# Performance work log

Measured on AMD Instinct MI355X. Metric: run time of the kernel, lower is better.

Reference implementation:

```python
import jax, jax.numpy as jnp
import numpy as np

N = 100000      # nodes
E = 600000      # directed edges (reciprocal pairs)
D_NODE = 128    # node feature dim (== hidden, required by torch.where broadcast)
D_BOND = 16     # bond feature dim
HID = 128       # hidden size
DEPTH = 3       # message passing depth


def setup_inputs() -> dict:
    key = jax.random.key(0)
    ks = jax.random.split(key, 8)
    x = jax.random.normal(ks[0], (N, D_NODE), jnp.float32)
    # build edges as reciprocal pairs: edge 2i = (u,v), edge 2i+1 = (v,u)
    half = E // 2
    u = jax.random.randint(ks[1], (half,), 0, N)
    v = jax.random.randint(ks[2], (half,), 0, N)
    src = jnp.stack([u, v], axis=1).reshape(-1)
    dst = jnp.stack([v, u], axis=1).reshape(-1)
    edge_index = jnp.stack([src, dst])          # [2, E]
    rev_edge_index = jnp.arange(E) ^ 1           # reverse edge of 2i is 2i+1
    edge_attr = jax.random.normal(ks[3], (E, D_BOND), jnp.float32)
    # learned params (Linear: y = x @ W + b)
    s_i = 1.0 / np.sqrt(D_NODE + D_BOND)
    s_h = 1.0 / np.sqrt(HID)
    s_o = 1.0 / np.sqrt(D_NODE + HID)
    W_i = jax.random.normal(ks[4], (D_NODE + D_BOND, HID), jnp.float32) * s_i
    b_i = jnp.zeros((HID,), jnp.float32)
    W_h = jax.random.normal(ks[5], (HID, HID), jnp.float32) * s_h
    b_h = jnp.zeros((HID,), jnp.float32)
    W_o = jax.random.normal(ks[6], (D_NODE + HID, HID), jnp.float32) * s_o
    b_o = jnp.zeros((HID,), jnp.float32)
    return dict(x=x, edge_attr=edge_attr, W_i=W_i, b_i=b_i, W_h=W_h, b_h=b_h,
                W_o=W_o, b_o=b_o, edge_index=edge_index,
                rev_edge_index=rev_edge_index)


def reference(x, edge_attr, W_i, b_i, W_h, b_h, W_o, b_o,
              edge_index, rev_edge_index):
    src, dst = edge_index[0], edge_index[1]
    # H_0 = relu(W_i([x[src]; edge_attr]))
    H0 = jax.nn.relu(jnp.concatenate([x[src], edge_attr], axis=1) @ W_i + b_i)
    H = H0
    for _ in range(DEPTH - 1):
        # message: scatter-sum over dst, gather by src, subtract reverse edge
        agg = jax.ops.segment_sum(H, dst, num_segments=N)   # [N, HID]
        M = agg[src] - H[rev_edge_index]                    # [E, HID]
        # update: relu(H0 + W_h(M))   (dropout is identity in eval)
        H = jax.nn.relu(H0 + M @ W_h + b_h)
    # final node aggregation
    Mn = jax.ops.segment_sum(H, dst, num_segments=N)        # [N, HID]
    Mn = jnp.where(jnp.sum(Mn, axis=1, keepdims=True) == 0, x, Mn)
    out = jax.nn.relu(jnp.concatenate([x, Mn], axis=1) @ W_o + b_o)  # [N, HID]
    return out
```

## Files before the change

kernel.cpp:

```cpp
#include <hip/hip_runtime.h>
#include <hip/hip_bf16.h>

#define N_NODES 100000
#define N_EDGES 600000
#define HID 128
#define D_BOND 16
#define NB_CHUNKS 98

typedef __attribute__((ext_vector_type(8))) short bf16x8;
typedef __attribute__((ext_vector_type(4))) float f32x4;

__device__ __forceinline__ float bf2f(unsigned int u) {
    return __uint_as_float((u & 0xffffu) << 16);
}
__device__ __forceinline__ unsigned short f2bf(float f) {
    unsigned int x = __float_as_uint(f);
    x += 0x7fffu + ((x >> 16) & 1u);
    return (unsigned short)(x >> 16);
}
__device__ __forceinline__ unsigned int pk2(float a, float b) {
    return (unsigned int)f2bf(a) | ((unsigned int)f2bf(b) << 16);
}

template<int STRIDE, int XM>
__device__ __forceinline__ void stw(unsigned char* tile, int row, int byte, uint4 v) {
    *reinterpret_cast<uint4*>(tile + ((row * STRIDE + byte) ^ ((row & XM) << 4))) = v;
}
template<int STRIDE, int XM>
__device__ __forceinline__ uint4 ldw(const unsigned char* tile, int row, int byte) {
    return *reinterpret_cast<const uint4*>(tile + ((row * STRIDE + byte) ^ ((row & XM) << 4)));
}
template<int STRIDE, int XM>
__device__ __forceinline__ bf16x8 lda(const unsigned char* tile, int row, int byte) {
    return *reinterpret_cast<const bf16x8*>(tile + ((row * STRIDE + byte) ^ ((row & XM) << 4)));
}
template<int STRIDE, int XM>
__device__ __forceinline__ void st2w(unsigned char* tile, int row, int col, unsigned short v) {
    *reinterpret_cast<unsigned short*>(tile + ((row * STRIDE + col * 2) ^ ((row & XM) << 4))) = v;
}

__device__ __forceinline__ bf16x8 ifrag(int l, int shift) {
    bf16x8 b;
    const int target = (l & 15) + shift;
#pragma unroll
    for (int j = 0; j < 8; ++j)
        b[j] = (short)((((l >> 4) * 8 + j) == target) ? 0x3F80 : 0);
    return b;
}

__global__ __launch_bounds__(256) void k_hist(const int* __restrict__ dst,
                                              int* __restrict__ cnt) {
    int e = blockIdx.x * 256 + threadIdx.x;
    if (e < N_EDGES) atomicAdd(&cnt[dst[e]], 1);
}

__global__ __launch_bounds__(256) void k_blocksum(const int* __restrict__ cnt,
                                                  int* __restrict__ bsum) {
    __shared__ int red[256];
    const int b = blockIdx.x, t = threadIdx.x;
    const int base = b * 1024 + t * 4;
    int s = 0;
#pragma unroll
    for (int i = 0; i < 4; ++i) { int n = base + i; if (n < N_NODES) s += cnt[n]; }
    red[t] = s; __syncthreads();
    for (int o = 128; o > 0; o >>= 1) { if (t < o) red[t] += red[t + o]; __syncthreads(); }
    if (t == 0) bsum[b] = red[0];
}

__global__ __launch_bounds__(128) void k_scan_bsum(const int* __restrict__ bsum,
                                                   int* __restrict__ boff,
                                                   int* __restrict__ rowptr) {
    __shared__ int s[128];
    const int t = threadIdx.x;
    const int v = (t < NB_CHUNKS) ? bsum[t] : 0;
    s[t] = v; __syncthreads();
    for (int o = 1; o < 128; o <<= 1) {
        int add = 0; if (t >= o) add = s[t - o];
        __syncthreads();
        s[t] += add; __syncthreads();
    }
    if (t < NB_CHUNKS) boff[t] = s[t] - v;
    if (t == 0) rowptr[N_NODES] = N_EDGES;
}

__global__ __launch_bounds__(256) void k_scan_chunk(const int* __restrict__ cnt,
                                                    const int* __restrict__ boff,
                                                    int* __restrict__ rowptr,
                                                    int* __restrict__ wpos) {
    __shared__ int s[256];
    const int b = blockIdx.x, t = threadIdx.x;
    const int base = b * 1024 + t * 4;
    int v[4]; int ts = 0;
#pragma unroll
    for (int i = 0; i < 4; ++i) { int n = base + i; v[i] = (n < N_NODES) ? cnt[n] : 0; ts += v[i]; }
    s[t] = ts; __syncthreads();
    for (int o = 1; o < 256; o <<= 1) {
        int add = 0; if (t >= o) add = s[t - o];
        __syncthreads();
        s[t] += add; __syncthreads();
    }
    int run = s[t] - ts + boff[b];
#pragma unroll
    for (int i = 0; i < 4; ++i) {
        int n = base + i;
        if (n < N_NODES) { rowptr[n] = run; wpos[n] = run; }
        run += v[i];
    }
}

__global__ __launch_bounds__(256) void k_fill(const int* __restrict__ dst,
                                              int* __restrict__ wpos,
                                              int* __restrict__ eidx) {
    int e = blockIdx.x * 256 + threadIdx.x;
    if (e < N_EDGES) { int p = atomicAdd(&wpos[dst[e]], 1); eidx[p] = e; }
}

__global__ __launch_bounds__(256) void k_eacvt(const float* __restrict__ ea,
                                               unsigned short* __restrict__ eabf) {
    const size_t i = (size_t)(blockIdx.x * 256 + threadIdx.x) * 8;
    if (i >= (size_t)N_EDGES * D_BOND) return;
    const float4 v0 = *reinterpret_cast<const float4*>(&ea[i]);
    const float4 v1 = *reinterpret_cast<const float4*>(&ea[i + 4]);
    uint4 o;
    o.x = pk2(v0.x, v0.y); o.y = pk2(v0.z, v0.w);
    o.z = pk2(v1.x, v1.y); o.w = pk2(v1.z, v1.w);
    *reinterpret_cast<uint4*>(&eabf[i]) = o;
}

__global__ __launch_bounds__(256) void k_pack(const float* __restrict__ Wi,
                                              const float* __restrict__ Wh,
                                              const float* __restrict__ Wo,
                                              unsigned short* __restrict__ Pie,
                                              unsigned short* __restrict__ Pix,
                                              unsigned short* __restrict__ Ph,
                                              unsigned short* __restrict__ PhN,
                                              unsigned short* __restrict__ Po) {
    const int tid = blockIdx.x * 256 + threadIdx.x;
    const float* W; unsigned short* P; int Krows, base; float sgn = 1.f;
    if (tid < 512)        { W = Wi + 128 * HID; P = Pie; Krows = 16;  base = tid; }
    else if (tid < 2560)  { W = Wi; P = Pix; Krows = 128; base = tid - 512; }
    else if (tid < 4608)  { W = Wh; P = Ph;  Krows = 128; base = tid - 2560; }
    else if (tid < 6656)  { W = Wh; P = PhN; Krows = 128; base = tid - 4608; sgn = -1.f; }
    else                  { W = Wo; P = Po;  Krows = 256; base = tid - 6656; }
    const int l = base & 63, fc = base >> 6;
    const int c = fc & 7, kk = fc >> 3;
    const int col = c * 16 + (l & 15);
    const int k0 = kk * 32 + (l >> 4) * 8;
    float v[8];
#pragma unroll
    for (int j = 0; j < 8; ++j) {
        const int k = k0 + j;
        v[j] = (k < Krows) ? sgn * W[(size_t)k * HID + col] : 0.f;
    }
    uint4 o;
    o.x = pk2(v[0], v[1]); o.y = pk2(v[2], v[3]);
    o.z = pk2(v[4], v[5]); o.w = pk2(v[6], v[7]);
    *reinterpret_cast<uint4*>(&P[(size_t)base * 8]) = o;
}

__global__ __launch_bounds__(256) void k_xw(const float* __restrict__ x,
                                            const unsigned short* __restrict__ Pix,
                                            void* __restrict__ xa) {
    __shared__ __align__(16) unsigned char tX[32 * 256];
    const int n0 = blockIdx.x * 32;
    const int t = threadIdx.x;
#pragma unroll
    for (int i = 0; i < 2; ++i) {
        const int f = t + 256 * i, row = f >> 4, u = f & 15;
        const float* xp = &x[(size_t)(n0 + row) * HID + u * 8];
        const float4 v0 = *reinterpret_cast<const float4*>(xp);
        const float4 v1 = *reinterpret_cast<const float4*>(xp + 4);
        uint4 o;
        o.x = pk2(v0.x, v0.y); o.y = pk2(v0.z, v0.w);
        o.z = pk2(v1.x, v1.y); o.w = pk2(v1.z, v1.w);
        stw<256, 7>(tX, row, u * 16, o);
    }
    __syncthreads();
    const int w = t >> 6, l = t & 63;
    const int wr = w & 1, cb = (w >> 1) * 4;
    const int arow = 16 * wr + (l & 15);
    const int ko = (l >> 4) * 16;
    f32x4 acc[4] = {};
#pragma unroll
    for (int kk = 0; kk < 4; ++kk) {
        const bf16x8 a = lda<256, 7>(tX, arow, kk * 64 + ko);
#pragma unroll
        for (int c = 0; c < 4; ++c) {
            const bf16x8 b = *reinterpret_cast<const bf16x8*>(&Pix[(((kk * 8) + cb + c) * 64 + l) * 8]);
            acc[c] = __builtin_amdgcn_mfma_f32_16x16x32_bf16(a, b, acc[c], 0, 0, 0);
        }
    }
    __syncthreads();
    const int rbase = 16 * wr + 4 * (l >> 4);
#pragma unroll
    for (int c = 0; c < 4; ++c) {
        const int col = ((cb + c) << 4) | (l & 15);
#pragma unroll
        for (int rr = 0; rr < 4; ++rr)
            st2w<256, 7>(tX, rbase + rr, col, f2bf(acc[c][rr]));
    }
    __syncthreads();
#pragma unroll
    for (int i = 0; i < 2; ++i) {
        const int f = t + 256 * i, row = f >> 4, u = f & 15;
        *reinterpret_cast<uint4*>((char*)xa + (size_t)(n0 + row) * 512 + u * 16) =
            ldw<256, 7>(tX, row, u * 16);
    }
}

template<int STRIDE>
__device__ __forceinline__ void xw_init(const unsigned char* tX, int ar0, int ko,
                                        int cb, int l, f32x4 (&acc)[2][4]) {
    const bf16x8 bI0 = ifrag(l, 0), bI1 = ifrag(l, 16);
    const f32x4 z = {0.f, 0.f, 0.f, 0.f};
#pragma unroll
    for (int c = 0; c < 4; ++c) {
        const int fc = cb + c;
        const int wb = (fc == 7) ? 192 : 32 * fc;
        const bf16x8 bI = (fc == 7) ? bI1 : bI0;
        acc[0][c] = __builtin_amdgcn_mfma_f32_16x16x32_bf16(lda<STRIDE, 7>(tX, ar0, wb + ko), bI, z, 0, 0, 0);
        acc[1][c] = __builtin_amdgcn_mfma_f32_16x16x32_bf16(lda<STRIDE, 7>(tX, ar0 + 16, wb + ko), bI, z, 0, 0, 0);
    }
}

__global__ __launch_bounds__(256) void k_h0(const void* __restrict__ xa,
                                            const unsigned short* __restrict__ eabf,
                                            const unsigned short* __restrict__ Pie,
                                            const float* __restrict__ bi,
                                            const int* __restrict__ src,
                                            unsigned short* __restrict__ H) {
    __shared__ __align__(16) unsigned char tX[64 * 256];
    __shared__ __align__(16) unsigned char tE[64 * 64];
    __shared__ int s_src[64];
    const int e0 = blockIdx.x * 64;
    const int t = threadIdx.x;
    if (t < 64) s_src[t] = src[e0 + t];
    __syncthreads();
#pragma unroll
    for (int i = 0; i < 4; ++i) {
        const int f = t + 256 * i, e = f >> 4, u = f & 15;
        stw<256, 7>(tX, e, u * 16,
            *reinterpret_cast<const uint4*>((const char*)xa + (size_t)s_src[e] * 512 + u * 16));
    }
    {
        const int e = t >> 2, u = t & 3;
        uint4 v = make_uint4(0, 0, 0, 0);
        if (u < 2) v = *reinterpret_cast<const uint4*>(&eabf[(size_t)(e0 + e) * D_BOND + u * 8]);
        stw<64, 3>(tE, e, u * 16, v);
    }
    __syncthreads();
    const int w = t >> 6, l = t & 63;
    const int cb = (w & 1) * 4, wr0 = (w >> 1) * 2;
    const int ar0 = 16 * wr0 + (l & 15);
    const int ko = (l >> 4) * 16;
    f32x4 acc[2][4];
    xw_init<256>(tX, ar0, ko, cb, l, acc);
    {
        const bf16x8 a0 = lda<64, 3>(tE, ar0, ko);
        const bf16x8 a1 = lda<64, 3>(tE, ar0 + 16, ko);
#pragma unroll
        for (int c = 0; c < 4; ++c) {
            const bf16x8 b = *reinterpret_cast<const bf16x8*>(&Pie[((cb + c) * 64 + l) * 8]);
            acc[0][c] = __builtin_amdgcn_mfma_f32_16x16x32_bf16(a0, b, acc[0][c], 0, 0, 0);
            acc[1][c] = __builtin_amdgcn_mfma_f32_16x16x32_bf16(a1, b, acc[1][c], 0, 0, 0);
        }
    }
    __syncthreads();
#pragma unroll
    for (int r = 0; r < 2; ++r) {
        const int rbase = 16 * (wr0 + r) + 4 * (l >> 4);
#pragma unroll
        for (int c = 0; c < 4; ++c) {
            const int col = ((cb + c) << 4) | (l & 15);
            const float bv = bi[col];
#pragma unroll
            for (int rr = 0; rr < 4; ++rr)
                st2w<256, 7>(tX, rbase + rr, col, f2bf(fmaxf(acc[r][c][rr] + bv, 0.f)));
        }
    }
    __syncthreads();
#pragma unroll
    for (int i = 0; i < 4; ++i) {
        const int f = t + 256 * i, row = f >> 4, u = f & 15;
        *reinterpret_cast<uint4*>(&H[(size_t)(e0 + row) * HID + u * 8]) = ldw<256, 7>(tX, row, u * 16);
    }
}

__global__ __launch_bounds__(256) void k_agg(const unsigned short* __restrict__ H,
                                             const int* __restrict__ rowptr,
                                             const int* __restrict__ eidx,
                                             void* __restrict__ xa) {
    const int wid = (blockIdx.x * 256 + threadIdx.x) >> 6;
    const int lane = threadIdx.x & 63;
    if (wid >= N_NODES) return;
    const int beg = rowptr[wid], end = rowptr[wid + 1];
    float a0 = 0.f, a1 = 0.f;
    int j = beg;
    for (; j + 4 <= end; j += 4) {
        const int ei0 = eidx[j], ei1 = eidx[j + 1], ei2 = eidx[j + 2], ei3 = eidx[j + 3];
        const unsigned int p0 = *reinterpret_cast<const unsigned int*>(&H[(size_t)ei0 * HID + lane * 2]);
        const unsigned int p1 = *reinterpret_cast<const unsigned int*>(&H[(size_t)ei1 * HID + lane * 2]);
        const unsigned int p2 = *reinterpret_cast<const unsigned int*>(&H[(size_t)ei2 * HID + lane * 2]);
        const unsigned int p3 = *reinterpret_cast<const unsigned int*>(&H[(size_t)ei3 * HID + lane * 2]);
        a0 += bf2f(p0) + bf2f(p1) + bf2f(p2) + bf2f(p3);
        a1 += bf2f(p0 >> 16) + bf2f(p1 >> 16) + bf2f(p2 >> 16) + bf2f(p3 >> 16);
    }
    for (; j < end; ++j) {
        const int e = eidx[j];
        const unsigned int p = *reinterpret_cast<const unsigned int*>(&H[(size_t)e * HID + lane * 2]);
        a0 += bf2f(p);
        a1 += bf2f(p >> 16);
    }
    *reinterpret_cast<unsigned int*>((char*)xa + (size_t)wid * 512 + 256 + lane * 4) = pk2(a0, a1);
}

__global__ __launch_bounds__(256) void k_msg(const void* __restrict__ xa,
                                             const unsigned short* __restrict__ eabf,
                                             const unsigned short* __restrict__ Pie,
                                             const float* __restrict__ bi,
                                             const unsigned short* __restrict__ Ph,
                                             const unsigned short* __restrict__ PhN,
                                             const float* __restrict__ bh,
                                             const int* __restrict__ src,
                                             unsigned short* H) {
    __shared__ __align__(16) unsigned char tA[64 * 512];
    __shared__ __align__(16) unsigned char tH[64 * 256];
    __shared__ __align__(16) unsigned char tE[64 * 64];
    __shared__ int s_src[64];
    const int e0 = blockIdx.x * 64;
    const int t = threadIdx.x;
    if (t < 64) s_src[t] = src[e0 + t];
    __syncthreads();

#pragma unroll
    for (int i = 0; i < 8; ++i) {
        const int f = t + 256 * i, e = f >> 5, u = f & 31;
        stw<512, 7>(tA, e, u * 16,
            *reinterpret_cast<const uint4*>((const char*)xa + (size_t)s_src[e] * 512 + u * 16));
    }
#pragma unroll
    for (int i = 0; i < 4; ++i) {
        const int f = t + 256 * i, e = f >> 4, u = f & 15;
        stw<256, 7>(tH, e, u * 16,
            *reinterpret_cast<const uint4*>(&H[(size_t)((e0 + e) ^ 1) * HID + u * 8]));
    }
    {
        const int e = t >> 2, u = t & 3;
        uint4 v = make_uint4(0, 0, 0, 0);
        if (u < 2) v = *reinterpret_cast<const uint4*>(&eabf[(size_t)(e0 + e) * D_BOND + u * 8]);
        stw<64, 3>(tE, e, u * 16, v);
    }
    __syncthreads();

    const int w = t >> 6, l = t & 63;
    const int cb = (w & 1) * 4, wr0 = (w >> 1) * 2;
    const int ar0 = 16 * wr0 + (l & 15);
    const int ko = (l >> 4) * 16;

    f32x4 acc[2][4];
    xw_init<512>(tA, ar0, ko, cb, l, acc);
    {
        const bf16x8 a0 = lda<64, 3>(tE, ar0, ko);
        const bf16x8 a1 = lda<64, 3>(tE, ar0 + 16, ko);
#pragma unroll
        for (int c = 0; c < 4; ++c) {
            const bf16x8 b = *reinterpret_cast<const bf16x8*>(&Pie[((cb + c) * 64 + l) * 8]);
            acc[0][c] = __builtin_amdgcn_mfma_f32_16x16x32_bf16(a0, b, acc[0][c], 0, 0, 0);
            acc[1][c] = __builtin_amdgcn_mfma_f32_16x16x32_bf16(a1, b, acc[1][c], 0, 0, 0);
        }
    }
#pragma unroll
    for (int r = 0; r < 2; ++r)
#pragma unroll
        for (int c = 0; c < 4; ++c) {
            const float bv = bi[((cb + c) << 4) | (l & 15)];
#pragma unroll
            for (int rr = 0; rr < 4; ++rr) acc[r][c][rr] = fmaxf(acc[r][c][rr] + bv, 0.f);
        }
#pragma unroll
    for (int kk = 0; kk < 4; ++kk) {
        const bf16x8 a0 = lda<512, 7>(tA, ar0, 256 + kk * 64 + ko);
        const bf16x8 a1 = lda<512, 7>(tA, ar0 + 16, 256 + kk * 64 + ko);
#pragma unroll
        for (int c = 0; c < 4; ++c) {
            const bf16x8 b = *reinterpret_cast<const bf16x8*>(&Ph[(((kk * 8) + cb + c) * 64 + l) * 8]);
            acc[0][c] = __builtin_amdgcn_mfma_f32_16x16x32_bf16(a0, b, acc[0][c], 0, 0, 0);
            acc[1][c] = __builtin_amdgcn_mfma_f32_16x16x32_bf16(a1, b, acc[1][c], 0, 0, 0);
        }
    }
#pragma unroll
    for (int kk = 0; kk < 4; ++kk) {
        const bf16x8 a0 = lda<256, 7>(tH, ar0, kk * 64 + ko);
        const bf16x8 a1 = lda<256, 7>(tH, ar0 + 16, kk * 64 + ko);
#pragma unroll
        for (int c = 0; c < 4; ++c) {
            const bf16x8 b = *reinterpret_cast<const bf16x8*>(&PhN[(((kk * 8) + cb + c) * 64 + l) * 8]);
            acc[0][c] = __builtin_amdgcn_mfma_f32_16x16x32_bf16(a0, b, acc[0][c], 0, 0, 0);
            acc[1][c] = __builtin_amdgcn_mfma_f32_16x16x32_bf16(a1, b, acc[1][c], 0, 0, 0);
        }
    }
    __syncthreads();

#pragma unroll
    for (int r = 0; r < 2; ++r) {
        const int rbase = 16 * (wr0 + r) + 4 * (l >> 4);
#pragma unroll
        for (int c = 0; c < 4; ++c) {
            const int col = ((cb + c) << 4) | (l & 15);
            const float bv = bh[col];
#pragma unroll
            for (int rr = 0; rr < 4; ++rr)
                st2w<256, 7>(tH, rbase + rr, col, f2bf(fmaxf(acc[r][c][rr] + bv, 0.f)));
        }
    }
    __syncthreads();
#pragma unroll
    for (int i = 0; i < 4; ++i) {
        const int f = t + 256 * i, row = f >> 4, u = f & 15;
        *reinterpret_cast<uint4*>(&H[(size_t)(e0 + row) * HID + u * 8]) = ldw<256, 7>(tH, row, u * 16);
    }
}

__global__ __launch_bounds__(256) void k_out(const float* __restrict__ x,
                                             const void* xa,
                                             const int* __restrict__ cnt,
                                             const unsigned short* __restrict__ Po,
                                             const float* __restrict__ bo,
                                             float* out) {
    __shared__ __align__(16) unsigned char tile[32 * 512];
    __shared__ int s_cnt[32];
    const int n0 = blockIdx.x * 32;
    const int t = threadIdx.x;
    if (t < 32) s_cnt[t] = cnt[n0 + t];
    __syncthreads();
    for (int f = t; f < 1024; f += 256) {
        const int e = f >> 5, u = f & 31;
        uint4 o;
        if (u >= 16 && s_cnt[e] > 0) {
            o = *reinterpret_cast<const uint4*>((const char*)xa + (size_t)(n0 + e) * 512 + 256 + (u - 16) * 16);
        } else {
            const int k8 = (u & 15) * 8;
            const float* xp = &x[(size_t)(n0 + e) * HID + k8];
            const float4 v0 = *reinterpret_cast<const float4*>(xp);
            const float4 v1 = *reinterpret_cast<const float4*>(xp + 4);
            o.x = pk2(v0.x, v0.y); o.y = pk2(v0.z, v0.w);
            o.z = pk2(v1.x, v1.y); o.w = pk2(v1.z, v1.w);
        }
        stw<512, 7>(tile, e, u * 16, o);
    }
    __syncthreads();
    const int w = t >> 6, l = t & 63;
    const int wr = w & 1, cb = (w >> 1) * 4;
    const int arow = 16 * wr + (l & 15);
    const int ko = (l >> 4) * 16;
    f32x4 acc[4] = {};
#pragma unroll
    for (int kk = 0; kk < 8; ++kk) {
        const bf16x8 a = lda<512, 7>(tile, arow, kk * 64 + ko);
#pragma unroll
        for (int c = 0; c < 4; ++c) {
            const bf16x8 b = *reinterpret_cast<const bf16x8*>(&Po[(((kk * 8) + cb + c) * 64 + l) * 8]);
            acc[c] = __builtin_amdgcn_mfma_f32_16x16x32_bf16(a, b, acc[c], 0, 0, 0);
        }
    }
    const int frow = 16 * wr + 4 * (l >> 4);
#pragma unroll
    for (int c = 0; c < 4; ++c) {
        const int col = ((cb + c) << 4) | (l & 15);
        const float bias = bo[col];
#pragma unroll
        for (int r = 0; r < 4; ++r) {
            out[(size_t)(n0 + frow + r) * HID + col] = fmaxf(acc[c][r] + bias, 0.f);
        }
    }
}

extern "C" void kernel_launch(void* const* d_in, const int* in_sizes, int n_in,
                              void* d_out, int out_size, void* d_ws, size_t ws_size,
                              hipStream_t stream) {
    const float* x  = (const float*)d_in[0];
    const float* ea = (const float*)d_in[1];
    const float* Wi = (const float*)d_in[2];
    const float* bi = (const float*)d_in[3];
    const float* Wh = (const float*)d_in[4];
    const float* bh = (const float*)d_in[5];
    const float* Wo = (const float*)d_in[6];
    const float* bo = (const float*)d_in[7];
    const int* ei   = (const int*)d_in[8];
    const int* src  = ei;
    const int* dst  = ei + N_EDGES;

    char* ws = (char*)d_ws;
    size_t off = 0;
    auto alloc = [&](size_t bytes) -> void* {
        void* p = ws + off;
        off += (bytes + 255) & ~(size_t)255;
        return p;
    };
    unsigned short* H    = (unsigned short*)alloc((size_t)N_EDGES * HID * 2);
    unsigned short* eabf = (unsigned short*)alloc((size_t)N_EDGES * D_BOND * 2);
    int* cnt     = (int*)alloc((size_t)N_NODES * 4);
    int* rowptr  = (int*)alloc((size_t)(N_NODES + 1) * 4);
    int* wpos    = (int*)alloc((size_t)N_NODES * 4);
    int* bsum    = (int*)alloc(512);
    int* boff    = (int*)alloc(512);
    int* eidx    = (int*)alloc((size_t)N_EDGES * 4);
    unsigned short* Pie = (unsigned short*)alloc(512 * 8 * 2);
    unsigned short* Pix = (unsigned short*)alloc(2048 * 8 * 2);
    unsigned short* Ph  = (unsigned short*)alloc(2048 * 8 * 2);
    unsigned short* PhN = (unsigned short*)alloc(2048 * 8 * 2);
    unsigned short* Po  = (unsigned short*)alloc(4096 * 8 * 2);
    void* xa = d_out;

    const int EB = (N_EDGES + 255) / 256;

    hipMemsetAsync(cnt, 0, (size_t)N_NODES * 4, stream);
    k_hist<<<EB, 256, 0, stream>>>(dst, cnt);
    k_blocksum<<<NB_CHUNKS, 256, 0, stream>>>(cnt, bsum);
    k_scan_bsum<<<1, 128, 0, stream>>>(bsum, boff, rowptr);
    k_scan_chunk<<<NB_CHUNKS, 256, 0, stream>>>(cnt, boff, rowptr, wpos);
    k_fill<<<EB, 256, 0, stream>>>(dst, wpos, eidx);

    k_eacvt<<<(N_EDGES * D_BOND / 8 + 255) / 256, 256, 0, stream>>>(ea, eabf);
    k_pack<<<42, 256, 0, stream>>>(Wi, Wh, Wo, Pie, Pix, Ph, PhN, Po);
    k_xw<<<N_NODES / 32, 256, 0, stream>>>(x, Pix, xa);

    k_h0<<<N_EDGES / 64, 256, 0, stream>>>(xa, eabf, Pie, bi, src, H);

    k_agg<<<N_NODES / 4, 256, 0, stream>>>(H, rowptr, eidx, xa);
    k_msg<<<N_EDGES / 64, 256, 0, stream>>>(xa, eabf, Pie, bi, Ph, PhN, bh, src, H);

    k_agg<<<N_NODES / 4, 256, 0, stream>>>(H, rowptr, eidx, xa);
    k_msg<<<N_EDGES / 64, 256, 0, stream>>>(xa, eabf, Pie, bi, Ph, PhN, bh, src, H);

    k_agg<<<N_NODES / 4, 256, 0, stream>>>(H, rowptr, eidx, xa);
    k_out<<<N_NODES / 32, 256, 0, stream>>>(x, xa, cnt, Po, bo, (float*)d_out);
}
```

Before: 625.8 us.

## Recompute H0 on the fly and drop the separate H0 materialization kernel

Removes the k_h0 kernel that wrote the full edge-level H0 tensor. A new k_agg0 rebuilds H0 per incoming edge from the precomputed x·W_i rows plus the bond features, and sums it straight into the node aggregate. The first k_msg variant recomputes H0 in shared memory and reads each edge's reverse by XOR-ing the row inside the 64-edge tile, since reciprocal edges are adjacent. The later variant loads H rows contiguously and does the same XOR in LDS instead of gathering globally. This saves a full edge-tensor write and read, at the cost of redundant scalar FMA work and uncoalesced fp32 edge_attr reads in k_agg0.

```diff
diff --git a/kernel.cpp b/kernel.cpp
--- a/kernel.cpp
+++ b/kernel.cpp
@@ -223,67 +223,43 @@
     }
 }
 
-__global__ __launch_bounds__(256) void k_h0(const void* __restrict__ xa,
-                                            const unsigned short* __restrict__ eabf,
-                                            const unsigned short* __restrict__ Pie,
-                                            const float* __restrict__ bi,
-                                            const int* __restrict__ src,
-                                            unsigned short* __restrict__ H) {
-    __shared__ __align__(16) unsigned char tX[64 * 256];
-    __shared__ __align__(16) unsigned char tE[64 * 64];
-    __shared__ int s_src[64];
-    const int e0 = blockIdx.x * 64;
-    const int t = threadIdx.x;
-    if (t < 64) s_src[t] = src[e0 + t];
-    __syncthreads();
-#pragma unroll
-    for (int i = 0; i < 4; ++i) {
-        const int f = t + 256 * i, e = f >> 4, u = f & 15;
-        stw<256, 7>(tX, e, u * 16,
-            *reinterpret_cast<const uint4*>((const char*)xa + (size_t)s_src[e] * 512 + u * 16));
-    }
-    {
-        const int e = t >> 2, u = t & 3;
-        uint4 v = make_uint4(0, 0, 0, 0);
-        if (u < 2) v = *reinterpret_cast<const uint4*>(&eabf[(size_t)(e0 + e) * D_BOND + u * 8]);
-        stw<64, 3>(tE, e, u * 16, v);
-    }
-    __syncthreads();
-    const int w = t >> 6, l = t & 63;
-    const int cb = (w & 1) * 4, wr0 = (w >> 1) * 2;
-    const int ar0 = 16 * wr0 + (l & 15);
-    const int ko = (l >> 4) * 16;
-    f32x4 acc[2][4];
-    xw_init<256>(tX, ar0, ko, cb, l, acc);
-    {
-        const bf16x8 a0 = lda<64, 3>(tE, ar0, ko);
-        const bf16x8 a1 = lda<64, 3>(tE, ar0 + 16, ko);
-#pragma unroll
-        for (int c = 0; c < 4; ++c) {
-            const bf16x8 b = *reinterpret_cast<const bf16x8*>(&Pie[((cb + c) * 64 + l) * 8]);
-            acc[0][c] = __builtin_amdgcn_mfma_f32_16x16x32_bf16(a0, b, acc[0][c], 0, 0, 0);
-            acc[1][c] = __builtin_amdgcn_mfma_f32_16x16x32_bf16(a1, b, acc[1][c], 0, 0, 0);
-        }
-    }
-    __syncthreads();
-#pragma unroll
-    for (int r = 0; r < 2; ++r) {
-        const int rbase = 16 * (wr0 + r) + 4 * (l >> 4);
-#pragma unroll
-        for (int c = 0; c < 4; ++c) {
-            const int col = ((cb + c) << 4) | (l & 15);
-            const float bv = bi[col];
-#pragma unroll
-            for (int rr = 0; rr < 4; ++rr)
-                st2w<256, 7>(tX, rbase + rr, col, f2bf(fmaxf(acc[r][c][rr] + bv, 0.f)));
-        }
-    }
-    __syncthreads();
-#pragma unroll
-    for (int i = 0; i < 4; ++i) {
-        const int f = t + 256 * i, row = f >> 4, u = f & 15;
-        *reinterpret_cast<uint4*>(&H[(size_t)(e0 + row) * HID + u * 8]) = ldw<256, 7>(tX, row, u * 16);
-    }
+__global__ __launch_bounds__(256) void k_agg0(const int* __restrict__ rowptr,
+                                              const int* __restrict__ eidx,
+                                              const int* __restrict__ src,
+                                              const float* __restrict__ ea,
+                                              const float* __restrict__ Wi,
+                                              const float* __restrict__ bi,
+                                              void* __restrict__ xa) {
+    const int wid = (blockIdx.x * 256 + threadIdx.x) >> 6;
+    const int lane = threadIdx.x & 63;
+    if (wid >= N_NODES) return;
+    const int c0 = lane * 2;
+    float w2x[16], w2y[16];
+#pragma unroll
+    for (int k = 0; k < 16; ++k) {
+        const float2 v = *reinterpret_cast<const float2*>(&Wi[(size_t)(128 + k) * HID + c0]);
+        w2x[k] = v.x; w2y[k] = v.y;
+    }
+    const float2 bv = *reinterpret_cast<const float2*>(&bi[c0]);
+    float a0 = 0.f, a1 = 0.f;
+    const int beg = rowptr[wid], end = rowptr[wid + 1];
+    for (int j = beg; j < end; ++j) {
+        const int e = eidx[j];
+        const int s = src[e];
+        const unsigned int xw = *reinterpret_cast<const unsigned int*>((const char*)xa + (size_t)s * 512 + lane * 4);
+        float h0 = bf2f(xw) + bv.x, h1 = bf2f(xw >> 16) + bv.y;
+        const float* ep = &ea[(size_t)e * D_BOND];
+#pragma unroll
+        for (int k = 0; k < 16; ++k) {
+            const float ev = ep[k];
+            h0 = fmaf(ev, w2x[k], h0);
+            h1 = fmaf(ev, w2y[k], h1);
+        }
+        h0 = fmaxf(h0, 0.f); h1 = fmaxf(h1, 0.f);
+        a0 += bf2f((unsigned int)f2bf(h0));
+        a1 += bf2f((unsigned int)f2bf(h1));
+    }
+    *reinterpret_cast<unsigned int*>((char*)xa + (size_t)wid * 512 + 256 + lane * 4) = pk2(a0, a1);
 }
 
 __global__ __launch_bounds__(256) void k_agg(const unsigned short* __restrict__ H,
@@ -314,6 +290,7 @@
     *reinterpret_cast<unsigned int*>((char*)xa + (size_t)wid * 512 + 256 + lane * 4) = pk2(a0, a1);
 }
 
+template<int FIRST>
 __global__ __launch_bounds__(256) void k_msg(const void* __restrict__ xa,
                                              const unsigned short* __restrict__ eabf,
                                              const unsigned short* __restrict__ Pie,
@@ -338,11 +315,13 @@
         stw<512, 7>(tA, e, u * 16,
             *reinterpret_cast<const uint4*>((const char*)xa + (size_t)s_src[e] * 512 + u * 16));
     }
-#pragma unroll
-    for (int i = 0; i < 4; ++i) {
-        const int f = t + 256 * i, e = f >> 4, u = f & 15;
-        stw<256, 7>(tH, e, u * 16,
-            *reinterpret_cast<const uint4*>(&H[(size_t)((e0 + e) ^ 1) * HID + u * 8]));
+    if (!FIRST) {
+#pragma unroll
+        for (int i = 0; i < 4; ++i) {
+            const int f = t + 256 * i, e = f >> 4, u = f & 15;
+            stw<256, 7>(tH, e, u * 16,
+                *reinterpret_cast<const uint4*>(&H[(size_t)(e0 + e) * HID + u * 8]));
+        }
     }
     {
         const int e = t >> 2, u = t & 3;
@@ -377,6 +356,20 @@
 #pragma unroll
             for (int rr = 0; rr < 4; ++rr) acc[r][c][rr] = fmaxf(acc[r][c][rr] + bv, 0.f);
         }
+    if (FIRST) {
+#pragma unroll
+        for (int r = 0; r < 2; ++r) {
+            const int rbase = 16 * (wr0 + r) + 4 * (l >> 4);
+#pragma unroll
+            for (int c = 0; c < 4; ++c) {
+                const int col = ((cb + c) << 4) | (l & 15);
+#pragma unroll
+                for (int rr = 0; rr < 4; ++rr)
+                    st2w<256, 7>(tH, rbase + rr, col, f2bf(acc[r][c][rr]));
+            }
+        }
+        __syncthreads();
+    }
 #pragma unroll
     for (int kk = 0; kk < 4; ++kk) {
         const bf16x8 a0 = lda<512, 7>(tA, ar0, 256 + kk * 64 + ko);
@@ -390,8 +383,8 @@
     }
 #pragma unroll
     for (int kk = 0; kk < 4; ++kk) {
-        const bf16x8 a0 = lda<256, 7>(tH, ar0, kk * 64 + ko);
-        const bf16x8 a1 = lda<256, 7>(tH, ar0 + 16, kk * 64 + ko);
+        const bf16x8 a0 = lda<256, 7>(tH, ar0 ^ 1, kk * 64 + ko);
+        const bf16x8 a1 = lda<256, 7>(tH, (ar0 + 16) ^ 1, kk * 64 + ko);
 #pragma unroll
         for (int c = 0; c < 4; ++c) {
             const bf16x8 b = *reinterpret_cast<const bf16x8*>(&PhN[(((kk * 8) + cb + c) * 64 + l) * 8]);
@@ -525,13 +518,11 @@
     k_pack<<<42, 256, 0, stream>>>(Wi, Wh, Wo, Pie, Pix, Ph, PhN, Po);
     k_xw<<<N_NODES / 32, 256, 0, stream>>>(x, Pix, xa);
 
-    k_h0<<<N_EDGES / 64, 256, 0, stream>>>(xa, eabf, Pie, bi, src, H);
+    k_agg0<<<N_NODES / 4, 256, 0, stream>>>(rowptr, eidx, src, ea, Wi, bi, xa);
+    k_msg<1><<<N_EDGES / 64, 256, 0, stream>>>(xa, eabf, Pie, bi, Ph, PhN, bh, src, H);
 
     k_agg<<<N_NODES / 4, 256, 0, stream>>>(H, rowptr, eidx, xa);
-    k_msg<<<N_EDGES / 64, 256, 0, stream>>>(xa, eabf, Pie, bi, Ph, PhN, bh, src, H);
-
-    k_agg<<<N_NODES / 4, 256, 0, stream>>>(H, rowptr, eidx, xa);
-    k_msg<<<N_EDGES / 64, 256, 0, stream>>>(xa, eabf, Pie, bi, Ph, PhN, bh, src, H);
+    k_msg<0><<<N_EDGES / 64, 256, 0, stream>>>(xa, eabf, Pie, bi, Ph, PhN, bh, src, H);
 
     k_agg<<<N_NODES / 4, 256, 0, stream>>>(H, rowptr, eidx, xa);
     k_out<<<N_NODES / 32, 256, 0, stream>>>(x, xa, cnt, Po, bo, (float*)d_out);
```

After: 682.0 us. +9.0%, slower.
